# Optimization experiments

Hardware: AMD Instinct MI355X
Metric: run time of the kernel (lower is better)

Reference implementation:

```python
import jax, jax.numpy as jnp
import numpy as np

N_EMBED = 1024
N_HEADS = 16
CTX = 2048
B, T = 4, 2048
HD = N_EMBED // N_HEADS


def setup_inputs() -> dict:
    key = jax.random.key(0)
    ks = jax.random.split(key, 5)
    scale = 1.0 / np.sqrt(N_EMBED)
    return {
        "x": jax.random.normal(ks[0], (B, T, N_EMBED), dtype=jnp.float32),
        "wq": jax.random.normal(ks[1], (N_EMBED, N_EMBED), dtype=jnp.float32) * scale,
        "wk": jax.random.normal(ks[2], (N_EMBED, N_EMBED), dtype=jnp.float32) * scale,
        "wv": jax.random.normal(ks[3], (N_EMBED, N_EMBED), dtype=jnp.float32) * scale,
        "wo": jax.random.normal(ks[4], (N_EMBED, N_EMBED), dtype=jnp.float32) * scale,
    }


def reference(x, wq, wk, wv, wo):
    b, t, c = x.shape
    # nn.Linear applies x @ W.T ; split heads -> [B, H, T, hd]
    def proj(w):
        return jnp.einsum("btc,dc->btd", x, w).reshape(b, t, N_HEADS, HD).transpose(0, 2, 1, 3)
    q, k, v = proj(wq), proj(wk), proj(wv)
    scores = jnp.einsum("bhqd,bhkd->bhqk", q, k) * (HD ** -0.5)
    causal = jnp.tril(jnp.ones((t, t), dtype=bool))
    scores = jnp.where(causal[None, None, :, :], scores, -jnp.inf)
    a = jax.nn.softmax(scores, axis=-1)
    o = jnp.einsum("bhqk,bhkd->bhqd", a, v)  # [B,H,T,hd]
    o = o.transpose(0, 2, 1, 3).reshape(b, t, c)
    return jnp.einsum("btc,dc->btd", o, wo)
```

## Files before the change

kernel.cpp:

```cpp
#include <hip/hip_runtime.h>
#include <stdint.h>


typedef __attribute__((ext_vector_type(8))) short bf16x8;
typedef __attribute__((ext_vector_type(4))) float f32x4;
typedef __attribute__((ext_vector_type(16))) float f32x16;
typedef unsigned short us;
typedef unsigned int u32;

#define LOG2E 1.4426950408889634f

#define GL2LDS16(g, l)                                                          \
  __builtin_amdgcn_global_load_lds(                                             \
      (const __attribute__((address_space(1))) unsigned int*)(g),               \
      (__attribute__((address_space(3))) unsigned int*)(l), 16, 0, 0)

__device__ inline us f2bf(float f) {
  union { float f; unsigned int u; } v; v.f = f;
  unsigned int u = v.u;
  u += 0x7FFFu + ((u >> 16) & 1u);
  return (us)(u >> 16);
}

__global__ void cast_all(const float* __restrict__ x,
                         const float* __restrict__ w0, const float* __restrict__ w1,
                         const float* __restrict__ w2, const float* __restrict__ w3,
                         us* __restrict__ xb, us* __restrict__ wbuf) {
  int i = (blockIdx.x * blockDim.x + threadIdx.x) * 8;
  const float* src;
  us* dst;
  float sc = 1.0f;
  if (i < (8 << 20)) {
    src = x + i; dst = xb + i;
  } else {
    int j = i - (8 << 20);
    int seg = j >> 20;
    int off = j & ((1 << 20) - 1);
    const float* w = (seg == 0) ? w0 : (seg == 1) ? w1 : (seg == 2) ? w2 : w3;
    if (seg == 0) sc = 0.125f * LOG2E;
    src = w + off; dst = wbuf + j;
  }
  float4 a = *reinterpret_cast<const float4*>(src);
  float4 b = *reinterpret_cast<const float4*>(src + 4);
  union { us u[8]; uint4 v; } o;
  o.u[0] = f2bf(a.x * sc); o.u[1] = f2bf(a.y * sc);
  o.u[2] = f2bf(a.z * sc); o.u[3] = f2bf(a.w * sc);
  o.u[4] = f2bf(b.x * sc); o.u[5] = f2bf(b.y * sc);
  o.u[6] = f2bf(b.z * sc); o.u[7] = f2bf(b.w * sc);
  *reinterpret_cast<uint4*>(dst) = o.v;
}

__global__ __launch_bounds__(256, 2) void gemm_qkv(
    const us* __restrict__ A, const us* __restrict__ Bw,
    us* __restrict__ QKV, us* __restrict__ Vt) {
  const int K = 1024, N = 3072;
  __shared__ __align__(16) us Al[128 * 64];
  __shared__ __align__(16) us Bl[128 * 64];
  const int tid = threadIdx.x;
  const int lane = tid & 63;
  const int w = tid >> 6;
  const int quad = lane >> 4;
  const int l16 = lane & 15;
  const int m0 = blockIdx.y * 128;
  const int n0 = blockIdx.x * 128;
  const int wm = w >> 1, wn = w & 1;
  const int srow_base = w * 8 + (lane >> 3);
  const int sunit = lane & 7;
  f32x4 acc[4][4] = {};

  for (int k0 = 0; k0 < K; k0 += 64) {
    __syncthreads();
#pragma unroll
    for (int it = 0; it < 4; ++it) {
      int row = it * 32 + srow_base;
      int gu = sunit ^ (row & 7);
      int base = __builtin_amdgcn_readfirstlane((it * 256 + w * 64) * 8);
      GL2LDS16(A + (size_t)(m0 + row) * K + k0 + gu * 8, &Al[base]);
      GL2LDS16(Bw + (size_t)(n0 + row) * K + k0 + gu * 8, &Bl[base]);
    }
    __syncthreads();
#pragma unroll
    for (int kk = 0; kk < 2; ++kk) {
      bf16x8 af[4], bfr[4];
#pragma unroll
      for (int mi = 0; mi < 4; ++mi) {
        int row = wm * 64 + mi * 16 + l16;
        af[mi] = *reinterpret_cast<const bf16x8*>(
            &Al[row * 64 + (((kk * 4 + quad) ^ (row & 7)) * 8)]);
      }
#pragma unroll
      for (int ni = 0; ni < 4; ++ni) {
        int row = wn * 64 + ni * 16 + l16;
        bfr[ni] = *reinterpret_cast<const bf16x8*>(
            &Bl[row * 64 + (((kk * 4 + quad) ^ (row & 7)) * 8)]);
      }
#pragma unroll
      for (int mi = 0; mi < 4; ++mi)
#pragma unroll
        for (int ni = 0; ni < 4; ++ni)
          acc[mi][ni] = __builtin_amdgcn_mfma_f32_16x16x32_bf16(af[mi], bfr[ni], acc[mi][ni], 0, 0, 0);
    }
  }

  if (n0 < 2048) {
#pragma unroll
    for (int mi = 0; mi < 4; ++mi)
#pragma unroll
      for (int ni = 0; ni < 4; ++ni)
#pragma unroll
        for (int r = 0; r < 4; ++r) {
          int row = m0 + wm * 64 + mi * 16 + quad * 4 + r;
          int col = n0 + wn * 64 + ni * 16 + l16;
          QKV[(size_t)row * N + col] = f2bf(acc[mi][ni][r]);
        }
  } else {
    const int bI = m0 >> 11;
    const int tbase = m0 & 2047;
#pragma unroll
    for (int mi = 0; mi < 4; ++mi)
#pragma unroll
      for (int ni = 0; ni < 4; ++ni)
#pragma unroll
        for (int r = 0; r < 4; ++r) {
          int krow = tbase + wm * 64 + mi * 16 + quad * 4 + r;
          int col = n0 + wn * 64 + ni * 16 + l16;
          int hh = (col - 2048) >> 6;
          int d = col & 63;
          Vt[((size_t)((bI * 16 + hh) * 64 + d)) * 2048 + krow] = f2bf(acc[mi][ni][r]);
        }
  }
}

__global__ __launch_bounds__(256, 2) void gemm_out(
    const us* __restrict__ A, const us* __restrict__ Bw,
    float* __restrict__ Cv, int M, int N, int K) {
  __shared__ __align__(16) us Al[128 * 64];
  __shared__ __align__(16) us Bl[128 * 64];
  const int tid = threadIdx.x;
  const int lane = tid & 63;
  const int w = tid >> 6;
  const int quad = lane >> 4;
  const int l16 = lane & 15;
  const int m0 = blockIdx.y * 128;
  const int n0 = blockIdx.x * 128;
  const int wm = w >> 1, wn = w & 1;
  const int srow_base = w * 8 + (lane >> 3);
  const int sunit = lane & 7;
  f32x4 acc[4][4] = {};

  for (int k0 = 0; k0 < K; k0 += 64) {
    __syncthreads();
#pragma unroll
    for (int it = 0; it < 4; ++it) {
      int row = it * 32 + srow_base;
      int gu = sunit ^ (row & 7);
      int base = __builtin_amdgcn_readfirstlane((it * 256 + w * 64) * 8);
      GL2LDS16(A + (size_t)(m0 + row) * K + k0 + gu * 8, &Al[base]);
      GL2LDS16(Bw + (size_t)(n0 + row) * K + k0 + gu * 8, &Bl[base]);
    }
    __syncthreads();
#pragma unroll
    for (int kk = 0; kk < 2; ++kk) {
      bf16x8 af[4], bfr[4];
#pragma unroll
      for (int mi = 0; mi < 4; ++mi) {
        int row = wm * 64 + mi * 16 + l16;
        af[mi] = *reinterpret_cast<const bf16x8*>(
            &Al[row * 64 + (((kk * 4 + quad) ^ (row & 7)) * 8)]);
      }
#pragma unroll
      for (int ni = 0; ni < 4; ++ni) {
        int row = wn * 64 + ni * 16 + l16;
        bfr[ni] = *reinterpret_cast<const bf16x8*>(
            &Bl[row * 64 + (((kk * 4 + quad) ^ (row & 7)) * 8)]);
      }
#pragma unroll
      for (int mi = 0; mi < 4; ++mi)
#pragma unroll
        for (int ni = 0; ni < 4; ++ni)
          acc[mi][ni] = __builtin_amdgcn_mfma_f32_16x16x32_bf16(af[mi], bfr[ni], acc[mi][ni], 0, 0, 0);
    }
  }

#pragma unroll
  for (int mi = 0; mi < 4; ++mi)
#pragma unroll
    for (int ni = 0; ni < 4; ++ni)
#pragma unroll
      for (int r = 0; r < 4; ++r) {
        int row = m0 + wm * 64 + mi * 16 + quad * 4 + r;
        int col = n0 + wn * 64 + ni * 16 + l16;
        Cv[(size_t)row * N + col] = acc[mi][ni][r];
      }
}

__global__ __launch_bounds__(256, 4) void attn(
    const us* __restrict__ QKV, const us* __restrict__ Vt,
    us* __restrict__ O) {
  __shared__ __align__(16) us Kb[2][64 * 64];
  __shared__ __align__(16) us Vb[2][64 * 64];
  const int bid = blockIdx.x;
  const int j16 = bid >> 6;
  const int grp = j16 >> 2, pos = j16 & 3;
  const int qt = (grp == 0) ? 15 - pos : (grp == 1) ? pos
               : (grp == 2) ? 11 - pos : 4 + pos;
  const int bh = bid & 63;
  const int b = bh >> 4, h = bh & 15;
  const int q0 = qt * 128;
  const int tid = threadIdx.x, lane = tid & 63, w = tid >> 6;
  const int l31 = lane & 31, hi = lane >> 5;
  const size_t rowbase = (size_t)b * 2048;
  const int qcol = h * 64;
  const int kcol = 1024 + h * 64;
  const int qw = q0 + w * 32;
  const int nT = 2 * qt + 2;

  const bf16x8 ones = {(short)0x3F80, (short)0x3F80, (short)0x3F80, (short)0x3F80,
                       (short)0x3F80, (short)0x3F80, (short)0x3F80, (short)0x3F80};

  bf16x8 qf[4];
#pragma unroll
  for (int ds = 0; ds < 4; ++ds)
    qf[ds] = *reinterpret_cast<const bf16x8*>(
        &QKV[(rowbase + qw + l31) * 3072 + qcol + ds * 16 + hi * 8]);

  f32x16 oacc[2] = {};
  f32x16 lacc = {};

  const int rr8 = w * 8 + (lane >> 3);
  const int uu = lane & 7;

  auto stage = [&](int kt, int buf) {
#pragma unroll
    for (int c = 0; c < 2; ++c) {
      int row = c * 32 + rr8;
      int gu = uu ^ (row & 7);
      int base = __builtin_amdgcn_readfirstlane((c * 32 + w * 8) * 64);
      GL2LDS16(QKV + (rowbase + kt * 64 + row) * 3072 + kcol + gu * 8,
               &Kb[buf][base]);
      GL2LDS16(Vt + ((size_t)(bh * 64 + row)) * 2048 + kt * 64 + gu * 8,
               &Vb[buf][base]);
    }
  };

  stage(0, 0);

  for (int kt = 0; kt < nT; ++kt) {
    asm volatile("s_waitcnt vmcnt(0)" ::: "memory");
    asm volatile("s_barrier" ::: "memory");
    if (kt + 1 < nT) stage(kt + 1, (kt + 1) & 1);
    const us* Kl = &Kb[kt & 1][0];
    const us* Vl = &Vb[kt & 1][0];

    const int kdiff = qw + 31 - kt * 64;
    if (kdiff < 0) continue;
    const int tmax = (kdiff >= 32) ? 2 : 1;
    const bool do_mask = (kt * 64 + 63) > qw;

    f32x16 s[2] = {};
#pragma unroll
    for (int t = 0; t < 2; ++t) {
      if (t < tmax) {
#pragma unroll
        for (int ds = 0; ds < 4; ++ds) {
          int row = t * 32 + l31;
          bf16x8 kf = *reinterpret_cast<const bf16x8*>(
              &Kl[row * 64 + (((ds * 2 + hi) ^ (row & 7)) * 8)]);
          s[t] = __builtin_amdgcn_mfma_f32_32x32x16_bf16(kf, qf[ds], s[t], 0, 0, 0);
        }
      }
    }

    u32 pa[4][4];
#pragma unroll
    for (int t = 0; t < 2; ++t) {
      if (t < tmax) {
        float p[16];
        if (do_mask) {
#pragma unroll
          for (int r = 0; r < 16; ++r) {
            float e = __builtin_amdgcn_exp2f(s[t][r]);
            int kg = kt * 64 + t * 32 + (r & 3) + ((r >> 2) << 3) + hi * 4;
            p[r] = (kg <= qw + l31) ? e : 0.f;
          }
        } else {
#pragma unroll
          for (int r = 0; r < 16; ++r) p[r] = __builtin_amdgcn_exp2f(s[t][r]);
        }
        u32 pk[4][2];
#pragma unroll
        for (int bb = 0; bb < 4; ++bb)
#pragma unroll
          for (int w2 = 0; w2 < 2; ++w2)
            asm("v_cvt_pk_bf16_f32 %0, %1, %2"
                : "=v"(pk[bb][w2])
                : "v"(p[4 * bb + 2 * w2]), "v"(p[4 * bb + 2 * w2 + 1]));
#pragma unroll
        for (int s2 = 0; s2 < 2; ++s2)
#pragma unroll
          for (int w2 = 0; w2 < 2; ++w2) {
            u32 a = pk[2 * s2][w2];
            u32 c = pk[2 * s2 + 1][w2];
            asm volatile("v_permlane32_swap_b32 %0, %1" : "+v"(a), "+v"(c));
            pa[t * 2 + s2][w2] = a;
            pa[t * 2 + s2][2 + w2] = c;
          }
      }
    }

#pragma unroll
    for (int ks = 0; ks < 4; ++ks) {
      if (ks < tmax * 2) {
        union { u32 u[4]; bf16x8 v; } pu;
        pu.u[0] = pa[ks][0]; pu.u[1] = pa[ks][1];
        pu.u[2] = pa[ks][2]; pu.u[3] = pa[ks][3];
        bf16x8 paf = pu.v;
        lacc = __builtin_amdgcn_mfma_f32_32x32x16_bf16(paf, ones, lacc, 0, 0, 0);
#pragma unroll
        for (int dt = 0; dt < 2; ++dt) {
          int row = dt * 32 + l31;
          bf16x8 vf = *reinterpret_cast<const bf16x8*>(
              &Vl[row * 64 + (((ks * 2 + hi) ^ (row & 7)) * 8)]);
          oacc[dt] = __builtin_amdgcn_mfma_f32_32x32x16_bf16(paf, vf, oacc[dt], 0, 0, 0);
        }
      }
    }
  }

  float inv[16];
#pragma unroll
  for (int r = 0; r < 16; ++r) inv[r] = 1.0f / lacc[r];
#pragma unroll
  for (int dt = 0; dt < 2; ++dt)
#pragma unroll
    for (int r = 0; r < 16; ++r) {
      int qg = qw + (r & 3) + ((r >> 2) << 3) + hi * 4;
      O[(rowbase + qg) * 1024 + qcol + dt * 32 + l31] = f2bf(oacc[dt][r] * inv[r]);
    }
}

extern "C" void kernel_launch(void* const* d_in, const int* in_sizes, int n_in,
                              void* d_out, int out_size, void* d_ws, size_t ws_size,
                              hipStream_t stream) {
  const float* x = (const float*)d_in[0];
  const float* wq = (const float*)d_in[1];
  const float* wk = (const float*)d_in[2];
  const float* wv = (const float*)d_in[3];
  const float* wo = (const float*)d_in[4];

  const int BT = 8192, E = 1024;
  const size_t NX = (size_t)BT * E;
  const size_t NW = (size_t)E * E;

  us* xb = (us*)d_ws;
  us* wbuf = xb + NX;
  us* QKV = wbuf + 4 * NW;
  us* VtB = QKV + (size_t)BT * 3 * E;
  us* Ob = xb;

  cast_all<<<(int)((NX + 4 * NW) / 8 / 256), 256, 0, stream>>>(x, wq, wk, wv, wo, xb, wbuf);

  gemm_qkv<<<dim3(24, 64), 256, 0, stream>>>(xb, wbuf, QKV, VtB);
  attn<<<1024, 256, 0, stream>>>(QKV, VtB, Ob);
  gemm_out<<<dim3(8, 64), 256, 0, stream>>>(Ob, wbuf + 3 * NW, (float*)d_out, BT, E, E);
}
```

Before: 252.8 us.

## Replace ones-MFMA row sums with scalar psum, fuse QK/PV per subtile, change swizzle

Drops the extra MFMA that multiplied P by a ones matrix to get softmax denominators. Each lane now accumulates its own exp values, combines halves with a permlane swap, and redistributes the reciprocal through a small shared array. The QK, exp and PV stages are interleaved per 32-key subtile to shorten live ranges, the LDS swizzle becomes an XOR pattern (row&7)^((row>>3)&3), and launch bounds drop from 4 to 3 blocks per CU. The denominators now come from the fp32 exp values rather than their bf16-rounded versions, and the lower occupancy hint may hide less latency.

```diff
diff --git a/kernel.cpp b/kernel.cpp
--- a/kernel.cpp
+++ b/kernel.cpp
@@ -194,11 +194,12 @@
       }
 }
 
-__global__ __launch_bounds__(256, 4) void attn(
+__global__ __launch_bounds__(256, 3) void attn(
     const us* __restrict__ QKV, const us* __restrict__ Vt,
     us* __restrict__ O) {
   __shared__ __align__(16) us Kb[2][64 * 64];
   __shared__ __align__(16) us Vb[2][64 * 64];
+  __shared__ float Ls[4][32];
   const int bid = blockIdx.x;
   const int j16 = bid >> 6;
   const int grp = j16 >> 2, pos = j16 & 3;
@@ -215,8 +216,7 @@
   const int qw = q0 + w * 32;
   const int nT = 2 * qt + 2;
 
-  const bf16x8 ones = {(short)0x3F80, (short)0x3F80, (short)0x3F80, (short)0x3F80,
-                       (short)0x3F80, (short)0x3F80, (short)0x3F80, (short)0x3F80};
+  const int mr = (l31 & 7) ^ ((l31 >> 3) & 3);
 
   bf16x8 qf[4];
 #pragma unroll
@@ -225,16 +225,17 @@
         &QKV[(rowbase + qw + l31) * 3072 + qcol + ds * 16 + hi * 8]);
 
   f32x16 oacc[2] = {};
-  f32x16 lacc = {};
+  float psum = 0.f;
 
   const int rr8 = w * 8 + (lane >> 3);
+  const int ms = (rr8 & 7) ^ ((rr8 >> 3) & 3);
   const int uu = lane & 7;
+  const int gu = uu ^ ms;
 
   auto stage = [&](int kt, int buf) {
 #pragma unroll
     for (int c = 0; c < 2; ++c) {
       int row = c * 32 + rr8;
-      int gu = uu ^ (row & 7);
       int base = __builtin_amdgcn_readfirstlane((c * 32 + w * 8) * 64);
       GL2LDS16(QKV + (rowbase + kt * 64 + row) * 3072 + kcol + gu * 8,
                &Kb[buf][base]);
@@ -257,36 +258,35 @@
     const int tmax = (kdiff >= 32) ? 2 : 1;
     const bool do_mask = (kt * 64 + 63) > qw;
 
-    f32x16 s[2] = {};
 #pragma unroll
     for (int t = 0; t < 2; ++t) {
       if (t < tmax) {
+        f32x16 s = {};
 #pragma unroll
         for (int ds = 0; ds < 4; ++ds) {
           int row = t * 32 + l31;
           bf16x8 kf = *reinterpret_cast<const bf16x8*>(
-              &Kl[row * 64 + (((ds * 2 + hi) ^ (row & 7)) * 8)]);
-          s[t] = __builtin_amdgcn_mfma_f32_32x32x16_bf16(kf, qf[ds], s[t], 0, 0, 0);
-        }
-      }
-    }
-
-    u32 pa[4][4];
-#pragma unroll
-    for (int t = 0; t < 2; ++t) {
-      if (t < tmax) {
+              &Kl[row * 64 + (((ds * 2 + hi) ^ mr) * 8)]);
+          s = __builtin_amdgcn_mfma_f32_32x32x16_bf16(kf, qf[ds], s, 0, 0, 0);
+        }
+
         float p[16];
         if (do_mask) {
 #pragma unroll
           for (int r = 0; r < 16; ++r) {
-            float e = __builtin_amdgcn_exp2f(s[t][r]);
+            float e = __builtin_amdgcn_exp2f(s[r]);
             int kg = kt * 64 + t * 32 + (r & 3) + ((r >> 2) << 3) + hi * 4;
             p[r] = (kg <= qw + l31) ? e : 0.f;
+            psum += p[r];
           }
         } else {
 #pragma unroll
-          for (int r = 0; r < 16; ++r) p[r] = __builtin_amdgcn_exp2f(s[t][r]);
-        }
+          for (int r = 0; r < 16; ++r) {
+            p[r] = __builtin_amdgcn_exp2f(s[r]);
+            psum += p[r];
+          }
+        }
+
         u32 pk[4][2];
 #pragma unroll
         for (int bb = 0; bb < 4; ++bb)
@@ -295,41 +295,45 @@
             asm("v_cvt_pk_bf16_f32 %0, %1, %2"
                 : "=v"(pk[bb][w2])
                 : "v"(p[4 * bb + 2 * w2]), "v"(p[4 * bb + 2 * w2 + 1]));
-#pragma unroll
-        for (int s2 = 0; s2 < 2; ++s2)
+
+#pragma unroll
+        for (int s2 = 0; s2 < 2; ++s2) {
+          u32 pa[4];
 #pragma unroll
           for (int w2 = 0; w2 < 2; ++w2) {
             u32 a = pk[2 * s2][w2];
             u32 c = pk[2 * s2 + 1][w2];
             asm volatile("v_permlane32_swap_b32 %0, %1" : "+v"(a), "+v"(c));
-            pa[t * 2 + s2][w2] = a;
-            pa[t * 2 + s2][2 + w2] = c;
+            pa[w2] = a;
+            pa[2 + w2] = c;
           }
-      }
-    }
-
-#pragma unroll
-    for (int ks = 0; ks < 4; ++ks) {
-      if (ks < tmax * 2) {
-        union { u32 u[4]; bf16x8 v; } pu;
-        pu.u[0] = pa[ks][0]; pu.u[1] = pa[ks][1];
-        pu.u[2] = pa[ks][2]; pu.u[3] = pa[ks][3];
-        bf16x8 paf = pu.v;
-        lacc = __builtin_amdgcn_mfma_f32_32x32x16_bf16(paf, ones, lacc, 0, 0, 0);
-#pragma unroll
-        for (int dt = 0; dt < 2; ++dt) {
-          int row = dt * 32 + l31;
-          bf16x8 vf = *reinterpret_cast<const bf16x8*>(
-              &Vl[row * 64 + (((ks * 2 + hi) ^ (row & 7)) * 8)]);
-          oacc[dt] = __builtin_amdgcn_mfma_f32_32x32x16_bf16(paf, vf, oacc[dt], 0, 0, 0);
-        }
-      }
-    }
-  }
-
+          union { u32 u[4]; bf16x8 v; } pu;
+          pu.u[0] = pa[0]; pu.u[1] = pa[1]; pu.u[2] = pa[2]; pu.u[3] = pa[3];
+          bf16x8 paf = pu.v;
+          int ks = t * 2 + s2;
+#pragma unroll
+          for (int dt = 0; dt < 2; ++dt) {
+            int row = dt * 32 + l31;
+            bf16x8 vf = *reinterpret_cast<const bf16x8*>(
+                &Vl[row * 64 + (((ks * 2 + hi) ^ mr) * 8)]);
+            oacc[dt] = __builtin_amdgcn_mfma_f32_32x32x16_bf16(paf, vf, oacc[dt], 0, 0, 0);
+          }
+        }
+      }
+    }
+  }
+
+  {
+    float a = psum, c = psum;
+    asm volatile("v_permlane32_swap_b32 %0, %1" : "+v"(a), "+v"(c));
+    float invl = 1.0f / (a + c);
+    if (!hi) Ls[w][l31] = invl;
+    asm volatile("s_waitcnt lgkmcnt(0)" ::: "memory");
+  }
   float inv[16];
 #pragma unroll
-  for (int r = 0; r < 16; ++r) inv[r] = 1.0f / lacc[r];
+  for (int r = 0; r < 16; ++r)
+    inv[r] = Ls[w][(r & 3) + ((r >> 2) << 3) + hi * 4];
 #pragma unroll
   for (int dt = 0; dt < 2; ++dt)
 #pragma unroll
```

Result: faster. 225.3 us (-10.9%).
